# Kernel tuning notes

Hardware: AMD Instinct MI355X
Metric: run time of the kernel (lower is better)

Reference implementation:

```python
import jax, jax.numpy as jnp
import numpy as np
from jax import lax

WINDOW = 9
N_INT = 1000
WMSE_WEIGHTS = np.array([1.0, 2.0, 5.0, 10.0, 30.0], dtype=np.float32)
WMSE_THRESH = np.array([0.5, 2.0, 5.0, 10.0], dtype=np.float32)
LOSS_W = np.array([1e-4, 1.0], dtype=np.float32)


def setup_inputs() -> dict:
    key = jax.random.key(0)
    k1, k2 = jax.random.split(key)
    shape = (4, 1, 128, 128)
    return {
        "prediction": jax.random.normal(k1, shape, dtype=jnp.float32),
        "target": jax.random.normal(k2, shape, dtype=jnp.float32),
    }


def _box_mean(x, win):
    # Equivalent to the original shift-and-accumulate running mean: box sum over
    # in-bounds neighbors (edge-corrected mean). x: [B, 1, H, W].
    pad = win // 2
    k = jnp.ones((1, 1, win, win), x.dtype)
    num = lax.conv_general_dilated(x, k, (1, 1), [(pad, pad), (pad, pad)])
    ones = jnp.ones((1, 1) + x.shape[-2:], x.dtype)
    den = lax.conv_general_dilated(ones, k, (1, 1), [(pad, pad), (pad, pad)])
    return num / den


def _wmse(pred, tgt):
    # Threshold-weighted MSE: weight chosen by the largest threshold <= target.
    w = jnp.full_like(tgt, WMSE_WEIGHTS[0])
    for i in range(len(WMSE_THRESH)):
        w = jnp.where(tgt >= WMSE_THRESH[i], WMSE_WEIGHTS[i + 1], w)
    return jnp.mean(w * (pred - tgt) ** 2)


def _crps(pred, tgt, n):
    # Deterministic CRPS via numeric integration over n points spanning the
    # global data range: integral (H(x - pred) - H(x - tgt))^2 dx per pixel.
    lo = jnp.minimum(pred.min(), tgt.min())
    hi = jnp.maximum(pred.max(), tgt.max())
    x = jnp.linspace(lo, hi, n)
    dx = (hi - lo) / (n - 1)
    p = pred.reshape(-1)
    t = tgt.reshape(-1)
    Fp = x[:, None] >= p[None, :]  # [N_INT, n_pixels]
    Ft = x[:, None] >= t[None, :]
    sq = (Fp ^ Ft).astype(pred.dtype)  # (Fp - Ft)^2 for 0/1 indicators
    return jnp.mean(sq.sum(axis=0) * dx)


def reference(prediction, target):
    pred_dist = prediction - _box_mean(prediction, WINDOW)
    tgt_dist = target - _box_mean(target, WINDOW)
    wmse = _wmse(prediction, target)
    crps = _crps(pred_dist, tgt_dist, N_INT)
    return LOSS_W[0] * wmse + LOSS_W[1] * crps
```

## Files before the change

### kernel.cpp

```cpp
#include <hip/hip_runtime.h>


__global__ __launch_bounds__(256) void SPL_kA(const float* __restrict__ pred,
                                              const float* __restrict__ tgt,
                                              float* __restrict__ part,
                                              float2* __restrict__ dist) {
    __shared__ float sP[1280], sT[1280];
    __shared__ float vsP[256], vsT[256];
    __shared__ float red[12];

    int b = blockIdx.x;
    int t = threadIdx.x;
    int m  = b >> 6;
    int r2 = (b & 63) << 1;
    const float* p = pred + (m << 14);
    const float* q = tgt  + (m << 14);

#pragma unroll
    for (int s = 0; s < 5; ++s) {
        int k   = t + s * 256;
        int rr  = k >> 7;
        int cc  = k & 127;
        int grw = r2 - 4 + rr;
        bool ok = (unsigned)grw < 128u;
        sP[k] = ok ? p[(grw << 7) + cc] : 0.f;
        sT[k] = ok ? q[(grw << 7) + cc] : 0.f;
    }
    __syncthreads();

    int orow = t >> 7;
    int col  = t & 127;
    int row  = r2 + orow;

    float vp = 0.f, vt = 0.f;
    int vb = orow * 128 + col;
#pragma unroll
    for (int di = 0; di < 9; ++di) {
        vp += sP[vb + di * 128];
        vt += sT[vb + di * 128];
    }
    vsP[t] = vp; vsT[t] = vt;
    __syncthreads();

    float sp = 0.f, st = 0.f;
    int rbase = t & ~127;
#pragma unroll
    for (int dj = -4; dj <= 4; ++dj) {
        int jj = col + dj;
        if ((unsigned)jj < 128u) { sp += vsP[rbase + jj]; st += vsT[rbase + jj]; }
    }

    int   rc  = min(row, 4) + min(127 - row, 4) + 1;
    int   cn  = min(col, 4) + min(127 - col, 4) + 1;
    float den = (float)(rc * cn);
    float pv  = sP[(orow + 4) * 128 + col];
    float tv  = sT[(orow + 4) * 128 + col];
    float pd  = pv - sp / den;
    float td  = tv - st / den;

    dist[(b << 8) + t] = make_float2(pd, td);

    float w = 1.f;
    if (tv >= 0.5f) w = 2.f;
    if (tv >= 2.f)  w = 5.f;
    if (tv >= 5.f)  w = 10.f;
    if (tv >= 10.f) w = 30.f;
    float d  = pv - tv;
    float s  = w * d * d;
    float mn = fminf(pd, td);
    float mx = fmaxf(pd, td);

    for (int o = 32; o > 0; o >>= 1) {
        s  += __shfl_down(s, o, 64);
        mn  = fminf(mn, __shfl_down(mn, o, 64));
        mx  = fmaxf(mx, __shfl_down(mx, o, 64));
    }
    int lane = t & 63, wid = t >> 6;
    if (lane == 0) { red[wid] = s; red[4 + wid] = mn; red[8 + wid] = mx; }
    __syncthreads();
    if (t == 0) {
        part[b]       = red[0] + red[1] + red[2] + red[3];
        part[256 + b] = fminf(fminf(red[4], red[5]), fminf(red[6], red[7]));
        part[512 + b] = fmaxf(fmaxf(red[8], red[9]), fmaxf(red[10], red[11]));
    }
}

__global__ __launch_bounds__(1024) void SPL_kB(const float* __restrict__ part,
                                               const float4* __restrict__ dist4,
                                               float* __restrict__ out) {
    __shared__ float rs[16], rmn[16], rmx[16];
    __shared__ int   rci[16];
    __shared__ float bc[3];

    int t = threadIdx.x;
    int lane = t & 63, wid = t >> 6;

    float s = 0.f, mn = 3.4e38f, mx = -3.4e38f;
    if (t < 256) { s = part[t]; mn = part[256 + t]; mx = part[512 + t]; }
    for (int o = 32; o > 0; o >>= 1) {
        s  += __shfl_down(s, o, 64);
        mn  = fminf(mn, __shfl_down(mn, o, 64));
        mx  = fmaxf(mx, __shfl_down(mx, o, 64));
    }
    if (lane == 0) { rs[wid] = s; rmn[wid] = mn; rmx[wid] = mx; }
    __syncthreads();
    if (t == 0) {
        float ss = 0.f, m1 = 3.4e38f, m2 = -3.4e38f;
        for (int i = 0; i < 16; ++i) {
            ss += rs[i]; m1 = fminf(m1, rmn[i]); m2 = fmaxf(m2, rmx[i]);
        }
        bc[0] = m1; bc[1] = m2; bc[2] = ss;
    }
    __syncthreads();

    float lo = bc[0], hi = bc[1];
    float dx = (hi - lo) / 999.0f;
    float inv_dx = 1.0f / dx;

    int cnt = 0;
#pragma unroll 4
    for (int it = 0; it < 32; ++it) {
        float4 d = dist4[it * 1024 + t];
        float a0 = fminf(d.x, d.y), b0 = fmaxf(d.x, d.y);
        float a1 = fminf(d.z, d.w), b1 = fmaxf(d.z, d.w);
        int ka0 = (int)ceilf((a0 - lo) * inv_dx);
        int kb0 = (int)ceilf((b0 - lo) * inv_dx);
        int ka1 = (int)ceilf((a1 - lo) * inv_dx);
        int kb1 = (int)ceilf((b1 - lo) * inv_dx);
        ka0 = max(ka0, 0); kb0 = min(kb0, 1000);
        ka1 = max(ka1, 0); kb1 = min(kb1, 1000);
        cnt += max(kb0 - ka0, 0) + max(kb1 - ka1, 0);
    }
    for (int o = 32; o > 0; o >>= 1) cnt += __shfl_down(cnt, o, 64);
    if (lane == 0) rci[wid] = cnt;
    __syncthreads();
    if (t == 0) {
        long long tot = 0;
        for (int i = 0; i < 16; ++i) tot += rci[i];
        float  wmse = bc[2] * (1.0f / 65536.0f);
        double crps = (double)tot * (double)dx / 65536.0;
        out[0] = 1e-4f * wmse + (float)crps;
    }
}

extern "C" void kernel_launch(void* const* d_in, const int* in_sizes, int n_in,
                              void* d_out, int out_size, void* d_ws, size_t ws_size,
                              hipStream_t stream) {
    const float* pred = (const float*)d_in[0];
    const float* tgt  = (const float*)d_in[1];
    float*  part = (float*)d_ws;
    float2* dist = (float2*)(part + 768);
    float*  out  = (float*)d_out;

    SPL_kA<<<256, 256, 0, stream>>>(pred, tgt, part, dist);
    SPL_kB<<<1, 1024, 0, stream>>>(part, (const float4*)dist, out);
}
```

Before: 68.06 us.

## Fuse two kernels into one cooperative kernel with grid syncs

Merges the stencil/partials kernel and the single-block CRPS counting kernel into one cooperative launch. Grid-wide syncs replace the kernel boundary, and each thread keeps its own pd/td in registers, so the dist buffer is no longer written and re-read. The final reduction is spread across all blocks instead of one 1024-thread block. The trade-off is two grid.sync barriers and the overhead of a cooperative launch.

```diff
diff --git a/kernel.cpp b/kernel.cpp
--- a/kernel.cpp
+++ b/kernel.cpp
@@ -1,13 +1,20 @@
 #include <hip/hip_runtime.h>
+#include <hip/hip_cooperative_groups.h>
+
+namespace cg = cooperative_groups;
 
 
-__global__ __launch_bounds__(256) void SPL_kA(const float* __restrict__ pred,
-                                              const float* __restrict__ tgt,
-                                              float* __restrict__ part,
-                                              float2* __restrict__ dist) {
+__global__ __launch_bounds__(256) void SPL_fused(const float* __restrict__ pred,
+                                                 const float* __restrict__ tgt,
+                                                 float* __restrict__ part,
+                                                 float* __restrict__ out) {
     __shared__ float sP[1280], sT[1280];
     __shared__ float vsP[256], vsT[256];
     __shared__ float red[12];
+    __shared__ int   redi[4];
+    __shared__ float bcast[2];
+
+    cg::grid_group grid = cg::this_grid();
 
     int b = blockIdx.x;
     int t = threadIdx.x;
@@ -58,8 +65,6 @@
     float pd  = pv - sp / den;
     float td  = tv - st / den;
 
-    dist[(b << 8) + t] = make_float2(pd, td);
-
     float w = 1.f;
     if (tv >= 0.5f) w = 2.f;
     if (tv >= 2.f)  w = 5.f;
@@ -83,63 +88,57 @@
         part[256 + b] = fminf(fminf(red[4], red[5]), fminf(red[6], red[7]));
         part[512 + b] = fmaxf(fmaxf(red[8], red[9]), fmaxf(red[10], red[11]));
     }
-}
 
-__global__ __launch_bounds__(1024) void SPL_kB(const float* __restrict__ part,
-                                               const float4* __restrict__ dist4,
-                                               float* __restrict__ out) {
-    __shared__ float rs[16], rmn[16], rmx[16];
-    __shared__ int   rci[16];
-    __shared__ float bc[3];
+    grid.sync();
 
-    int t = threadIdx.x;
-    int lane = t & 63, wid = t >> 6;
-
-    float s = 0.f, mn = 3.4e38f, mx = -3.4e38f;
-    if (t < 256) { s = part[t]; mn = part[256 + t]; mx = part[512 + t]; }
+    float mn2 = part[256 + t];
+    float mx2 = part[512 + t];
     for (int o = 32; o > 0; o >>= 1) {
-        s  += __shfl_down(s, o, 64);
-        mn  = fminf(mn, __shfl_down(mn, o, 64));
-        mx  = fmaxf(mx, __shfl_down(mx, o, 64));
+        mn2 = fminf(mn2, __shfl_down(mn2, o, 64));
+        mx2 = fmaxf(mx2, __shfl_down(mx2, o, 64));
     }
-    if (lane == 0) { rs[wid] = s; rmn[wid] = mn; rmx[wid] = mx; }
+    if (lane == 0) { red[4 + wid] = mn2; red[8 + wid] = mx2; }
     __syncthreads();
     if (t == 0) {
-        float ss = 0.f, m1 = 3.4e38f, m2 = -3.4e38f;
-        for (int i = 0; i < 16; ++i) {
-            ss += rs[i]; m1 = fminf(m1, rmn[i]); m2 = fmaxf(m2, rmx[i]);
-        }
-        bc[0] = m1; bc[1] = m2; bc[2] = ss;
+        bcast[0] = fminf(fminf(red[4], red[5]), fminf(red[6], red[7]));
+        bcast[1] = fmaxf(fmaxf(red[8], red[9]), fmaxf(red[10], red[11]));
     }
     __syncthreads();
-
-    float lo = bc[0], hi = bc[1];
+    float lo = bcast[0], hi = bcast[1];
     float dx = (hi - lo) / 999.0f;
     float inv_dx = 1.0f / dx;
 
-    int cnt = 0;
-#pragma unroll 4
-    for (int it = 0; it < 32; ++it) {
-        float4 d = dist4[it * 1024 + t];
-        float a0 = fminf(d.x, d.y), b0 = fmaxf(d.x, d.y);
-        float a1 = fminf(d.z, d.w), b1 = fmaxf(d.z, d.w);
-        int ka0 = (int)ceilf((a0 - lo) * inv_dx);
-        int kb0 = (int)ceilf((b0 - lo) * inv_dx);
-        int ka1 = (int)ceilf((a1 - lo) * inv_dx);
-        int kb1 = (int)ceilf((b1 - lo) * inv_dx);
-        ka0 = max(ka0, 0); kb0 = min(kb0, 1000);
-        ka1 = max(ka1, 0); kb1 = min(kb1, 1000);
-        cnt += max(kb0 - ka0, 0) + max(kb1 - ka1, 0);
-    }
+    float a0 = fminf(pd, td);
+    float b0 = fmaxf(pd, td);
+    int ka = (int)ceilf((a0 - lo) * inv_dx);
+    int kb = (int)ceilf((b0 - lo) * inv_dx);
+    ka = max(ka, 0); kb = min(kb, 1000);
+    int cnt = max(kb - ka, 0);
+
     for (int o = 32; o > 0; o >>= 1) cnt += __shfl_down(cnt, o, 64);
-    if (lane == 0) rci[wid] = cnt;
+    if (lane == 0) redi[wid] = cnt;
     __syncthreads();
     if (t == 0) {
-        long long tot = 0;
-        for (int i = 0; i < 16; ++i) tot += rci[i];
-        float  wmse = bc[2] * (1.0f / 65536.0f);
-        double crps = (double)tot * (double)dx / 65536.0;
-        out[0] = 1e-4f * wmse + (float)crps;
+        ((int*)part)[768 + b] = redi[0] + redi[1] + redi[2] + redi[3];
+    }
+
+    grid.sync();
+
+    if (b == 0) {
+        int   c  = ((const int*)part)[768 + t];
+        float ss = part[t];
+        for (int o = 32; o > 0; o >>= 1) {
+            c  += __shfl_down(c, o, 64);
+            ss += __shfl_down(ss, o, 64);
+        }
+        if (lane == 0) { redi[wid] = c; red[wid] = ss; }
+        __syncthreads();
+        if (t == 0) {
+            long long tot = (long long)redi[0] + redi[1] + redi[2] + redi[3];
+            float  wmse = (red[0] + red[1] + red[2] + red[3]) * (1.0f / 65536.0f);
+            double crps = (double)tot * (double)dx / 65536.0;
+            out[0] = 1e-4f * wmse + (float)crps;
+        }
     }
 }
 
@@ -148,10 +147,9 @@
                               hipStream_t stream) {
     const float* pred = (const float*)d_in[0];
     const float* tgt  = (const float*)d_in[1];
-    float*  part = (float*)d_ws;
-    float2* dist = (float2*)(part + 768);
-    float*  out  = (float*)d_out;
+    float* part = (float*)d_ws;
+    float* out  = (float*)d_out;
 
-    SPL_kA<<<256, 256, 0, stream>>>(pred, tgt, part, dist);
-    SPL_kB<<<1, 1024, 0, stream>>>(part, (const float4*)dist, out);
+    void* args[] = { (void*)&pred, (void*)&tgt, (void*)&part, (void*)&out };
+    hipLaunchCooperativeKernel((void*)SPL_fused, dim3(256), dim3(256), args, 0, stream);
 }
```

After: 118.7 us. 1.74x slower.
